# Optimization experiments

Hardware: AMD Instinct MI355X
Metric: run time of the kernel (lower is better)

The kernel has to match this reference:

```python
import jax, jax.numpy as jnp
import numpy as np

B, S, E, H, C = 64, 512, 768, 768, 9
Q_GCE = 0.7
TAU = 0.7
IGNORE = -100


def setup_inputs() -> dict:
    key = jax.random.key(0)
    k_h, k_w1, k_w2, k_lab, k_drop = jax.random.split(key, 5)
    hidden = jax.random.normal(k_h, (B, S, E), dtype=jnp.float32)
    W1 = jax.random.normal(k_w1, (E, H), dtype=jnp.float32) * (1.0 / np.sqrt(E))
    b1 = jnp.zeros((H,), dtype=jnp.float32)
    W2 = jax.random.normal(k_w2, (H, C), dtype=jnp.float32) * (1.0 / np.sqrt(H))
    b2 = jnp.zeros((C,), dtype=jnp.float32)
    labels = jax.random.randint(k_lab, (B, S), 0, C, dtype=jnp.int64 if jax.config.jax_enable_x64 else jnp.int32)
    drop = jax.random.uniform(k_drop, (B, S)) < 0.1
    labels = jnp.where(drop, IGNORE, labels)
    return {"hidden": hidden, "W1": W1, "b1": b1, "W2": W2, "b2": b2,
            "labels": labels, "epoch": 5}


def reference(hidden, W1, b1, W2, b2, labels, epoch):
    # head: Linear -> Tanh -> Linear (dropout is identity at eval)
    h = jnp.tanh(jnp.einsum('bse,eh->bsh', hidden, W1) + b1)
    logit = jnp.einsum('bsh,hc->bsc', h, W2) + b2
    probs = jax.nn.softmax(logit, axis=2)  # [B,S,C]

    mask = labels != IGNORE
    safe_labels = jnp.where(mask, labels, 0)
    # p_i = probs[i, labels[i]] gathered for every token
    p = jnp.take_along_axis(probs, safe_labels[..., None], axis=2)[..., 0]  # [B,S]
    # GCE weight: w=1 for epoch<=2, else 1 if p>tau else 0 (constant wrt grads)
    w = jnp.where(epoch <= 2, 1.0, jnp.where(p > TAU, 1.0, 0.0))
    w = jax.lax.stop_gradient(w) * mask.astype(probs.dtype)
    loss = jnp.sum(w * (1.0 - jnp.power(p, Q_GCE)) / Q_GCE)
    return probs, loss
```

## Files before the change

### kernel.cpp

```cpp
#include <hip/hip_runtime.h>
#include <hip/hip_bf16.h>
#include <stdint.h>

#define E_ 768
#define H_ 768
#define C_ 9
#define M_TOTAL 32768
#define BM_ 64

typedef __attribute__((ext_vector_type(8))) __bf16 bf16x8;
typedef __attribute__((ext_vector_type(4))) float f32x4;
typedef __attribute__((ext_vector_type(4))) int i32x4;

static_assert(sizeof(bf16x8) == 16, "bf16x8 must be 16B");

__device__ __forceinline__ unsigned short f2bf(float f) {
    __hip_bfloat16 h = __float2bfloat16(f);
    return __builtin_bit_cast(unsigned short, h);
}

__global__ void prep_kernel(const float* __restrict__ W1, const float* __restrict__ W2,
                            unsigned short* __restrict__ W1f, unsigned short* __restrict__ W2f,
                            float* __restrict__ loss_out)
{
    int b = blockIdx.x;
    int n = threadIdx.x;
    if (b < 768) {
        int k = b;
        float v = W1[k * H_ + n];
        int ntile = n >> 4;
        int t = k >> 5;
        int lane = (n & 15) + 16 * ((k >> 3) & 3);
        int j = k & 7;
        W1f[((ntile * 24 + t) * 64 + lane) * 8 + j] = f2bf(v);
    } else {
        for (int it = 0; it < 16; ++it) {
            int tid = it * 768 + n;
            int j    = tid & 7;
            int lane = (tid >> 3) & 63;
            int t    = tid >> 9;
            int cls  = lane & 15;
            int k = t * 32 + (lane >> 4) * 8 + j;
            W2f[tid] = (cls < C_) ? f2bf(W2[k * C_ + cls]) : (unsigned short)0;
        }
        if (n == 0) *loss_out = 0.0f;
    }
}

__launch_bounds__(1024, 4)
__global__ void fused_head_kernel(const float* __restrict__ hidden,
                                  const unsigned short* __restrict__ W1f,
                                  const float* __restrict__ b1,
                                  const unsigned short* __restrict__ W2f,
                                  const float* __restrict__ b2,
                                  const int* __restrict__ labels,
                                  const int* __restrict__ epoch_p,
                                  float* __restrict__ probs,
                                  float* __restrict__ loss)
{
    __shared__ unsigned short Ash[24 * 4 * 512];

    const int tid  = threadIdx.x;
    const int w    = tid >> 6;
    const int lane = tid & 63;
    const int tok0 = blockIdx.x * BM_;
    const int c16  = lane & 15;
    const int q    = lane >> 4;

    const f32x4* hsrc = (const f32x4*)(hidden + (size_t)tok0 * E_);
    const int tkA = tid >> 5;
    const int fq  = tid & 31;
    const int t_l = fq >> 3;
    const int jj  = (fq & 1) * 4;
    const int q2s = (fq >> 1) & 3;

    f32x4 rg0, rg1;
    auto issue = [&](int c) {
        rg0 = __builtin_nontemporal_load(hsrc + (size_t)tkA * 192 + c * 32 + fq);
        rg1 = __builtin_nontemporal_load(hsrc + (size_t)(tkA + 32) * 192 + c * 32 + fq);
    };
    auto stage = [&](int bsel) {
        unsigned short* bufp = &Ash[bsel * 8192];
        {
            int lnf = (tkA & 15) + 16 * q2s;
            int mt  = tkA >> 4;
            ushort4 pk = { f2bf(rg0[0]), f2bf(rg0[1]), f2bf(rg0[2]), f2bf(rg0[3]) };
            *(ushort4*)(&bufp[((t_l * 4 + mt) * 64 + lnf) * 8 + jj]) = pk;
        }
        {
            int tk  = tkA + 32;
            int lnf = (tk & 15) + 16 * q2s;
            int mt  = tk >> 4;
            ushort4 pk = { f2bf(rg1[0]), f2bf(rg1[1]), f2bf(rg1[2]), f2bf(rg1[3]) };
            *(ushort4*)(&bufp[((t_l * 4 + mt) * 64 + lnf) * 8 + jj]) = pk;
        }
    };

    issue(0);

    const unsigned short* Wp = W1f + (size_t)(w * 3 * 24) * 512 + lane * 8;
    bf16x8 bA[3], bB[3];
    #pragma unroll
    for (int i = 0; i < 3; ++i)
        bA[i] = __builtin_bit_cast(bf16x8, *(const i32x4*)(Wp + (i * 24 + 0) * 512));
    #pragma unroll
    for (int i = 0; i < 3; ++i)
        bB[i] = __builtin_bit_cast(bf16x8, *(const i32x4*)(Wp + (i * 24 + 1) * 512));

    const f32x4 zero4 = {0.0f, 0.0f, 0.0f, 0.0f};
    f32x4 acc[4][3];
    #pragma unroll
    for (int mt = 0; mt < 4; ++mt)
        #pragma unroll
        for (int nt = 0; nt < 3; ++nt) acc[mt][nt] = zero4;

    stage(0);
    asm volatile("s_waitcnt lgkmcnt(0)\ns_barrier" ::: "memory");

    #pragma unroll
    for (int c = 0; c < 6; ++c) {
        const unsigned short* bufp = &Ash[(c & 1) * 8192];
        if (c < 5) issue(c + 1);
        #pragma unroll
        for (int tl = 0; tl < 2; ++tl) {
            const int tt = 2 * c + tl;
            {
                bf16x8 af[4];
                #pragma unroll
                for (int mt = 0; mt < 4; ++mt)
                    af[mt] = __builtin_bit_cast(bf16x8,
                        *(const i32x4*)(&bufp[(((2 * tl) * 4 + mt) * 64 + lane) * 8]));
                #pragma unroll
                for (int mt = 0; mt < 4; ++mt)
                    #pragma unroll
                    for (int nt = 0; nt < 3; ++nt)
                        acc[mt][nt] = __builtin_amdgcn_mfma_f32_16x16x32_bf16(
                            af[mt], bA[nt], acc[mt][nt], 0, 0, 0);
            }
            if (tt < 11) {
                #pragma unroll
                for (int i = 0; i < 3; ++i)
                    bA[i] = __builtin_bit_cast(bf16x8,
                        *(const i32x4*)(Wp + (i * 24 + 2 * tt + 2) * 512));
            }
            {
                bf16x8 af[4];
                #pragma unroll
                for (int mt = 0; mt < 4; ++mt)
                    af[mt] = __builtin_bit_cast(bf16x8,
                        *(const i32x4*)(&bufp[(((2 * tl + 1) * 4 + mt) * 64 + lane) * 8]));
                #pragma unroll
                for (int mt = 0; mt < 4; ++mt)
                    #pragma unroll
                    for (int nt = 0; nt < 3; ++nt)
                        acc[mt][nt] = __builtin_amdgcn_mfma_f32_16x16x32_bf16(
                            af[mt], bB[nt], acc[mt][nt], 0, 0, 0);
            }
            if (tt < 11) {
                #pragma unroll
                for (int i = 0; i < 3; ++i)
                    bB[i] = __builtin_bit_cast(bf16x8,
                        *(const i32x4*)(Wp + (i * 24 + 2 * tt + 3) * 512));
            }
        }
        if (c < 5) stage((c + 1) & 1);
        asm volatile("s_waitcnt lgkmcnt(0)\ns_barrier" ::: "memory");
    }

    unsigned short* Hsh = &Ash[0];
    #pragma unroll
    for (int i = 0; i < 3; ++i) {
        int col = w * 48 + i * 16 + c16;
        float b1v = b1[col];
        int t2 = col >> 5;
        int q2 = (col >> 3) & 3;
        int j  = col & 7;
        #pragma unroll
        for (int mt = 0; mt < 4; ++mt) {
            #pragma unroll
            for (int r = 0; r < 4; ++r) {
                float z = acc[mt][i][r] + b1v;
                float e = exp2f(z * 2.8853900817779268f);
                float th = 1.0f - 2.0f * __builtin_amdgcn_rcpf(e + 1.0f);
                int lanep = (q * 4 + r) + 16 * q2;
                Hsh[((t2 * 4 + mt) * 64 + lanep) * 8 + j] = f2bf(th);
            }
        }
    }
    asm volatile("s_waitcnt lgkmcnt(0)\ns_barrier" ::: "memory");

    if (w < 4) {
        f32x4 logit = zero4;
        #pragma unroll
        for (int t2 = 0; t2 < 24; ++t2) {
            bf16x8 ha = __builtin_bit_cast(bf16x8, *(const i32x4*)(&Hsh[((t2 * 4 + w) * 64 + lane) * 8]));
            bf16x8 wb = __builtin_bit_cast(bf16x8, *(const i32x4*)(W2f + ((size_t)t2 * 64 + lane) * 8));
            logit = __builtin_amdgcn_mfma_f32_16x16x32_bf16(ha, wb, logit, 0, 0, 0);
        }

        const bool valid = (c16 < C_);
        const float b2v = valid ? b2[c16] : 0.0f;
        const int ep = epoch_p[0];
        float lsum = 0.0f;
        #pragma unroll
        for (int r = 0; r < 4; ++r) {
            float l = valid ? (logit[r] + b2v) : -3.0e38f;
            float m = l;
            #pragma unroll
            for (int d = 1; d < 16; d <<= 1)
                m = fmaxf(m, __shfl_xor(m, d, 64));
            float e = valid ? exp2f((l - m) * 1.44269504f) : 0.0f;
            float s = e;
            #pragma unroll
            for (int d = 1; d < 16; d <<= 1)
                s += __shfl_xor(s, d, 64);
            float p = e / s;
            int row = tok0 + w * 16 + q * 4 + r;
            if (valid) __builtin_nontemporal_store(p, &probs[(size_t)row * C_ + c16]);
            int lab = labels[row];
            if (valid && lab == c16) {
                float wgt = (ep <= 2) ? 1.0f : ((p > 0.7f) ? 1.0f : 0.0f);
                if (wgt > 0.0f)
                    lsum += (1.0f - exp2f(0.7f * log2f(p))) * (1.0f / 0.7f);
            }
        }
        #pragma unroll
        for (int d = 1; d < 64; d <<= 1)
            lsum += __shfl_xor(lsum, d, 64);
        if (lane == 0) atomicAdd(loss, lsum);
    }
}

extern "C" void kernel_launch(void* const* d_in, const int* in_sizes, int n_in,
                              void* d_out, int out_size, void* d_ws, size_t ws_size,
                              hipStream_t stream)
{
    const float* hidden = (const float*)d_in[0];
    const float* W1     = (const float*)d_in[1];
    const float* b1     = (const float*)d_in[2];
    const float* W2     = (const float*)d_in[3];
    const float* b2     = (const float*)d_in[4];
    const int*   labels = (const int*)d_in[5];
    const int*   epoch  = (const int*)d_in[6];

    float* probs = (float*)d_out;
    float* loss  = probs + (size_t)M_TOTAL * C_;

    unsigned short* W1f = (unsigned short*)d_ws;
    unsigned short* W2f = W1f + 48 * 24 * 512;

    prep_kernel<<<769, 768, 0, stream>>>(W1, W2, W1f, W2f, loss);
    fused_head_kernel<<<M_TOTAL / BM_, 1024, 0, stream>>>(hidden, W1f, b1, W2f, b2,
                                                          labels, epoch, probs, loss);
}
```

Baseline: 219.5 us.

## Software-pipeline LDS A-fragment loads and raise MFMA wave priority in GEMM loop

The GEMM1 inner loop now double-buffers the A fragments in registers, prefetching the next k-tile's LDS reads while the current MFMAs run. It also moves the staging of the next chunk into LDS to the middle of the chunk instead of the end. MFMA blocks are wrapped in s_setprio to favour math issue. The aim is to hide LDS latency and shorten the barrier-bound tail of each chunk, at the cost of more vector registers, which may lower occupancy.

```diff
diff --git a/kernel.cpp b/kernel.cpp
--- a/kernel.cpp
+++ b/kernel.cpp
@@ -99,13 +99,13 @@
     issue(0);
 
     const unsigned short* Wp = W1f + (size_t)(w * 3 * 24) * 512 + lane * 8;
-    bf16x8 bA[3], bB[3];
+    bf16x8 b0[3], b1v_[3];
     #pragma unroll
     for (int i = 0; i < 3; ++i)
-        bA[i] = __builtin_bit_cast(bf16x8, *(const i32x4*)(Wp + (i * 24 + 0) * 512));
+        b0[i] = __builtin_bit_cast(bf16x8, *(const i32x4*)(Wp + (i * 24 + 0) * 512));
     #pragma unroll
     for (int i = 0; i < 3; ++i)
-        bB[i] = __builtin_bit_cast(bf16x8, *(const i32x4*)(Wp + (i * 24 + 1) * 512));
+        b1v_[i] = __builtin_bit_cast(bf16x8, *(const i32x4*)(Wp + (i * 24 + 1) * 512));
 
     const f32x4 zero4 = {0.0f, 0.0f, 0.0f, 0.0f};
     f32x4 acc[4][3];
@@ -116,62 +116,77 @@
 
     stage(0);
     asm volatile("s_waitcnt lgkmcnt(0)\ns_barrier" ::: "memory");
+
+    bf16x8 af[2][4];
+    {
+        const unsigned short* bufp = &Ash[0];
+        #pragma unroll
+        for (int mt = 0; mt < 4; ++mt)
+            af[0][mt] = __builtin_bit_cast(bf16x8,
+                *(const i32x4*)(&bufp[((0 * 4 + mt) * 64 + lane) * 8]));
+    }
 
     #pragma unroll
     for (int c = 0; c < 6; ++c) {
         const unsigned short* bufp = &Ash[(c & 1) * 8192];
         if (c < 5) issue(c + 1);
         #pragma unroll
-        for (int tl = 0; tl < 2; ++tl) {
-            const int tt = 2 * c + tl;
-            {
-                bf16x8 af[4];
+        for (int tl = 0; tl < 4; ++tl) {
+            const int tt = 4 * c + tl;
+            const int cur = tl & 1;
+            if (tl < 3) {
                 #pragma unroll
                 for (int mt = 0; mt < 4; ++mt)
-                    af[mt] = __builtin_bit_cast(bf16x8,
-                        *(const i32x4*)(&bufp[(((2 * tl) * 4 + mt) * 64 + lane) * 8]));
+                    af[cur ^ 1][mt] = __builtin_bit_cast(bf16x8,
+                        *(const i32x4*)(&bufp[(((tl + 1) * 4 + mt) * 64 + lane) * 8]));
+            }
+            __builtin_amdgcn_s_setprio(1);
+            if ((tt & 1) == 0) {
                 #pragma unroll
                 for (int mt = 0; mt < 4; ++mt)
                     #pragma unroll
                     for (int nt = 0; nt < 3; ++nt)
                         acc[mt][nt] = __builtin_amdgcn_mfma_f32_16x16x32_bf16(
-                            af[mt], bA[nt], acc[mt][nt], 0, 0, 0);
-            }
-            if (tt < 11) {
-                #pragma unroll
-                for (int i = 0; i < 3; ++i)
-                    bA[i] = __builtin_bit_cast(bf16x8,
-                        *(const i32x4*)(Wp + (i * 24 + 2 * tt + 2) * 512));
-            }
-            {
-                bf16x8 af[4];
+                            af[cur][mt], b0[nt], acc[mt][nt], 0, 0, 0);
+            } else {
                 #pragma unroll
                 for (int mt = 0; mt < 4; ++mt)
-                    af[mt] = __builtin_bit_cast(bf16x8,
-                        *(const i32x4*)(&bufp[(((2 * tl + 1) * 4 + mt) * 64 + lane) * 8]));
-                #pragma unroll
-                for (int mt = 0; mt < 4; ++mt)
                     #pragma unroll
                     for (int nt = 0; nt < 3; ++nt)
                         acc[mt][nt] = __builtin_amdgcn_mfma_f32_16x16x32_bf16(
-                            af[mt], bB[nt], acc[mt][nt], 0, 0, 0);
-            }
-            if (tt < 11) {
-                #pragma unroll
-                for (int i = 0; i < 3; ++i)
-                    bB[i] = __builtin_bit_cast(bf16x8,
-                        *(const i32x4*)(Wp + (i * 24 + 2 * tt + 3) * 512));
-            }
-        }
-        if (c < 5) stage((c + 1) & 1);
+                            af[cur][mt], b1v_[nt], acc[mt][nt], 0, 0, 0);
+            }
+            __builtin_amdgcn_s_setprio(0);
+            if (tt + 2 < 24) {
+                if ((tt & 1) == 0) {
+                    #pragma unroll
+                    for (int i = 0; i < 3; ++i)
+                        b0[i] = __builtin_bit_cast(bf16x8,
+                            *(const i32x4*)(Wp + (i * 24 + tt + 2) * 512));
+                } else {
+                    #pragma unroll
+                    for (int i = 0; i < 3; ++i)
+                        b1v_[i] = __builtin_bit_cast(bf16x8,
+                            *(const i32x4*)(Wp + (i * 24 + tt + 2) * 512));
+                }
+            }
+            if (tl == 1 && c < 5) stage((c + 1) & 1);
+        }
         asm volatile("s_waitcnt lgkmcnt(0)\ns_barrier" ::: "memory");
+        if (c < 5) {
+            const unsigned short* bufn = &Ash[((c + 1) & 1) * 8192];
+            #pragma unroll
+            for (int mt = 0; mt < 4; ++mt)
+                af[0][mt] = __builtin_bit_cast(bf16x8,
+                    *(const i32x4*)(&bufn[((0 * 4 + mt) * 64 + lane) * 8]));
+        }
     }
 
     unsigned short* Hsh = &Ash[0];
     #pragma unroll
     for (int i = 0; i < 3; ++i) {
         int col = w * 48 + i * 16 + c16;
-        float b1v = b1[col];
+        float b1b = b1[col];
         int t2 = col >> 5;
         int q2 = (col >> 3) & 3;
         int j  = col & 7;
@@ -179,7 +194,7 @@
         for (int mt = 0; mt < 4; ++mt) {
             #pragma unroll
             for (int r = 0; r < 4; ++r) {
-                float z = acc[mt][i][r] + b1v;
+                float z = acc[mt][i][r] + b1b;
                 float e = exp2f(z * 2.8853900817779268f);
                 float th = 1.0f - 2.0f * __builtin_amdgcn_rcpf(e + 1.0f);
                 int lanep = (q * 4 + r) + 16 * q2;
```

Result: faster. 214.6 us (-2.2%).
